# Kernel tuning notes

Hardware: AMD Instinct MI355X
Metric: run time of the kernel (lower is better)

## Reference

```python
import jax, jax.numpy as jnp
import numpy as np

K, A, DIM = 1024, 16384, 512


def setup_inputs() -> dict:
    key = jax.random.key(0)
    ks = jax.random.split(key, 8)
    B, H, W = 2048, 8, 8
    z_t = jax.random.randint(ks[0], (B, H, W), 0, K, dtype=jnp.int64)
    z_tp1 = jax.random.randint(ks[1], (B, H, W), 0, K, dtype=jnp.int64)
    embed_w = jax.random.normal(ks[2], (K, DIM), dtype=jnp.float32) * 0.02
    # MLP: Linear(2*dim -> dim), GELU, Linear(dim -> dim)
    lim1 = 1.0 / np.sqrt(2 * DIM)
    w1 = jax.random.uniform(ks[3], (2 * DIM, DIM), minval=-lim1, maxval=lim1, dtype=jnp.float32)
    b1 = jax.random.uniform(ks[4], (DIM,), minval=-lim1, maxval=lim1, dtype=jnp.float32)
    lim2 = 1.0 / np.sqrt(DIM)
    w2 = jax.random.uniform(ks[5], (DIM, DIM), minval=-lim2, maxval=lim2, dtype=jnp.float32)
    b2 = jax.random.uniform(ks[6], (DIM,), minval=-lim2, maxval=lim2, dtype=jnp.float32)
    codebook_w = jax.random.normal(ks[7], (A, DIM), dtype=jnp.float32) * 0.02
    return {"z_t": z_t, "z_tp1": z_tp1, "embed_w": embed_w, "w1": w1, "b1": b1,
            "w2": w2, "b2": b2, "codebook_w": codebook_w}


def reference(z_t, z_tp1, embed_w, w1, b1, w2, b2, codebook_w):
    B = z_t.shape[0]
    # embed int code grids and mean-pool over H*W tokens -> [B, dim]
    e_t = embed_w[z_t.reshape(B, -1)].mean(axis=1)
    e_tp1 = embed_w[z_tp1.reshape(B, -1)].mean(axis=1)
    h = jnp.concatenate([e_t, e_tp1], axis=-1)          # [B, 2*dim]
    h = jax.nn.gelu(h @ w1 + b1, approximate=False)
    e = h @ w2 + b2                                      # [B, dim]
    # VQ: squared L2 distance to each code, argmin, gather
    d2 = (jnp.sum(e * e, axis=1, keepdims=True)
          - 2.0 * e @ codebook_w.T
          + jnp.sum(codebook_w * codebook_w, axis=1)[None, :])  # [B, A]
    ids = jnp.argmin(d2, axis=1)                         # [B]
    q = codebook_w[ids]                                  # [B, dim]
    return ids, q
```

## Files before the change

kernel.cpp:

```cpp
#include <hip/hip_runtime.h>
#include <hip/hip_bf16.h>

#define TOK 64
#define DIMC 512

typedef __attribute__((ext_vector_type(8))) short v8s;
typedef __attribute__((ext_vector_type(4))) float v4f;

__device__ __forceinline__ unsigned int f2ord(float f) {
  unsigned int u = __float_as_uint(f);
  return (u & 0x80000000u) ? ~u : (u | 0x80000000u);
}

__device__ __forceinline__ float gelu_exact(float x) {
  return 0.5f * x * (1.0f + erff(x * 0.70710678118654752440f));
}

__device__ __forceinline__ unsigned short f2bf(float x) {
  unsigned int u = __float_as_uint(x);
  return (unsigned short)((u + 0x7FFFu + ((u >> 16) & 1u)) >> 16);
}
__device__ __forceinline__ float bf2f(unsigned short h) {
  return __uint_as_float((unsigned int)h << 16);
}

__device__ __forceinline__ void gl2lds16(const void* g, void* l) {
  __builtin_amdgcn_global_load_lds((const __attribute__((address_space(1))) void*)g,
                                   (__attribute__((address_space(3))) void*)l,
                                   16, 0, 0);
}

__global__ __launch_bounds__(256) void k_embed(const int* __restrict__ zt,
                                               const int* __restrict__ ztp,
                                               const float* __restrict__ emb,
                                               unsigned short* __restrict__ hh,
                                               unsigned short* __restrict__ hl,
                                               unsigned long long* __restrict__ rowmin) {
  const int b = blockIdx.x;
  const int tid = threadIdx.x;
  __shared__ int codes[128];
  if (tid < 64) codes[tid] = zt[b * TOK + tid];
  else if (tid < 128) codes[tid] = ztp[b * TOK + (tid - 64)];
  if (tid == 0) rowmin[b] = 0xFFFFFFFFFFFFFFFFull;
  __syncthreads();
  const int half = tid >> 7;
  const int c4 = tid & 127;
  const float4* emb4 = (const float4*)emb;
  float4 s = make_float4(0.f, 0.f, 0.f, 0.f);
  #pragma unroll 8
  for (int t = 0; t < TOK; t++) {
    const int code = codes[half * TOK + t];
    const float4 v = emb4[code * 128 + c4];
    s.x += v.x; s.y += v.y; s.z += v.z; s.w += v.w;
  }
  const float inv = 1.0f / 64.0f;
  float f[4] = {s.x * inv, s.y * inv, s.z * inv, s.w * inv};
  unsigned short hi[4], lo[4];
  #pragma unroll
  for (int i = 0; i < 4; i++) {
    hi[i] = f2bf(f[i]);
    lo[i] = f2bf(f[i] - bf2f(hi[i]));
  }
  const int off = b * 1024 + half * 512 + c4 * 4;
  *(ushort4*)&hh[off] = make_ushort4(hi[0], hi[1], hi[2], hi[3]);
  *(ushort4*)&hl[off] = make_ushort4(lo[0], lo[1], lo[2], lo[3]);
}

__global__ __launch_bounds__(256) void k_wprep(const float* __restrict__ w,
                                               unsigned short* __restrict__ wth,
                                               unsigned short* __restrict__ wtl,
                                               int Kd, int N) {
  __shared__ float t[32][33];
  const int k0 = blockIdx.x * 32, n0 = blockIdx.y * 32;
  const int c = threadIdx.x & 31, r = threadIdx.x >> 5;
  #pragma unroll
  for (int i = 0; i < 4; i++)
    t[r + i * 8][c] = w[(size_t)(k0 + r + i * 8) * N + n0 + c];
  __syncthreads();
  #pragma unroll
  for (int i = 0; i < 4; i++) {
    const float v = t[c][r + i * 8];
    const unsigned short hi = f2bf(v);
    const unsigned short lo = f2bf(v - bf2f(hi));
    wth[(size_t)(n0 + r + i * 8) * Kd + k0 + c] = hi;
    wtl[(size_t)(n0 + r + i * 8) * Kd + k0 + c] = lo;
  }
}

template <bool GELU>
__global__ __launch_bounds__(256) void k_gemm(const unsigned short* __restrict__ Ah_,
                                              const unsigned short* __restrict__ Al_,
                                              const unsigned short* __restrict__ Bh_,
                                              const unsigned short* __restrict__ Bl_,
                                              const float* __restrict__ bias,
                                              unsigned short* __restrict__ oh,
                                              unsigned short* __restrict__ ol,
                                              int Kd, int N) {
  __shared__ unsigned short Ahs[64 * 32];
  __shared__ unsigned short Als[64 * 32];
  __shared__ unsigned short Bhs[64 * 32];
  __shared__ unsigned short Bls[64 * 32];

  const int tid = threadIdx.x;
  const int lane = tid & 63;
  const int wid = tid >> 6;
  const int m0 = blockIdx.x * 64;
  const int n0 = blockIdx.y * 64;

  v4f acc[2][2];
  #pragma unroll
  for (int i = 0; i < 2; i++)
    #pragma unroll
    for (int j = 0; j < 2; j++) acc[i][j] = (v4f)(0.f);

  const unsigned short* gsrc;
  unsigned short* ldst;
  if (wid == 0)      { gsrc = Ah_ + (size_t)m0 * Kd; ldst = Ahs; }
  else if (wid == 1) { gsrc = Al_ + (size_t)m0 * Kd; ldst = Als; }
  else if (wid == 2) { gsrc = Bh_ + (size_t)n0 * Kd; ldst = Bhs; }
  else               { gsrc = Bl_ + (size_t)n0 * Kd; ldst = Bls; }

  const int srow = lane >> 2;
  const int sk = (lane & 3) * 8;
  const int wm = wid >> 1, wn = wid & 1;
  const int fr = lane & 15;
  const int fq = (lane >> 4) * 8;

  for (int k0 = 0; k0 < Kd; k0 += 32) {
    __syncthreads();
    #pragma unroll
    for (int j = 0; j < 4; j++)
      gl2lds16(gsrc + (size_t)(j * 16 + srow) * Kd + k0 + sk, ldst + j * 512);
    __syncthreads();

    v8s ah[2], al[2], bh[2], bl[2];
    #pragma unroll
    for (int t = 0; t < 2; t++) {
      const int ar = (wm * 32 + t * 16 + fr) * 32 + fq;
      const int br = (wn * 32 + t * 16 + fr) * 32 + fq;
      ah[t] = *(const v8s*)&Ahs[ar];
      al[t] = *(const v8s*)&Als[ar];
      bh[t] = *(const v8s*)&Bhs[br];
      bl[t] = *(const v8s*)&Bls[br];
    }
    #pragma unroll
    for (int mt = 0; mt < 2; mt++)
      #pragma unroll
      for (int nt = 0; nt < 2; nt++) {
        acc[mt][nt] = __builtin_amdgcn_mfma_f32_16x16x32_bf16(ah[mt], bh[nt], acc[mt][nt], 0, 0, 0);
        acc[mt][nt] = __builtin_amdgcn_mfma_f32_16x16x32_bf16(ah[mt], bl[nt], acc[mt][nt], 0, 0, 0);
        acc[mt][nt] = __builtin_amdgcn_mfma_f32_16x16x32_bf16(al[mt], bh[nt], acc[mt][nt], 0, 0, 0);
      }
  }

  const int col16 = lane & 15;
  const int q = lane >> 4;
  int colv[2]; float bv[2];
  #pragma unroll
  for (int nt = 0; nt < 2; nt++) {
    colv[nt] = n0 + wn * 32 + nt * 16 + col16;
    bv[nt] = bias[colv[nt]];
  }
  #pragma unroll
  for (int mt = 0; mt < 2; mt++)
    #pragma unroll
    for (int reg = 0; reg < 4; reg++) {
      const int row = m0 + wm * 32 + mt * 16 + q * 4 + reg;
      #pragma unroll
      for (int nt = 0; nt < 2; nt++) {
        float v = acc[mt][nt][reg] + bv[nt];
        if (GELU) v = gelu_exact(v);
        const unsigned short hi = f2bf(v);
        oh[(size_t)row * N + colv[nt]] = hi;
        ol[(size_t)row * N + colv[nt]] = f2bf(v - bf2f(hi));
      }
    }
}

__global__ __launch_bounds__(256) void k_cbprep(const float* __restrict__ cb,
                                                unsigned short* __restrict__ ch,
                                                unsigned short* __restrict__ cl,
                                                float* __restrict__ cnorm) {
  const int row = blockIdx.x * 4 + (threadIdx.x >> 6);
  const int lane = threadIdx.x & 63;
  const float4* cb4 = (const float4*)cb;
  const float4 va = cb4[row * 128 + lane * 2];
  const float4 vb = cb4[row * 128 + lane * 2 + 1];
  float s = va.x * va.x + va.y * va.y + va.z * va.z + va.w * va.w
          + vb.x * vb.x + vb.y * vb.y + vb.z * vb.z + vb.w * vb.w;
  float f[8] = {va.x, va.y, va.z, va.w, vb.x, vb.y, vb.z, vb.w};
  unsigned short hi[8], lo[8];
  #pragma unroll
  for (int i = 0; i < 8; i++) {
    hi[i] = f2bf(f[i]);
    lo[i] = f2bf(f[i] - bf2f(hi[i]));
  }
  ushort4* chp = (ushort4*)&ch[row * DIMC + lane * 8];
  ushort4* clp = (ushort4*)&cl[row * DIMC + lane * 8];
  chp[0] = make_ushort4(hi[0], hi[1], hi[2], hi[3]);
  chp[1] = make_ushort4(hi[4], hi[5], hi[6], hi[7]);
  clp[0] = make_ushort4(lo[0], lo[1], lo[2], lo[3]);
  clp[1] = make_ushort4(lo[4], lo[5], lo[6], lo[7]);
  #pragma unroll
  for (int off = 32; off > 0; off >>= 1) s += __shfl_down(s, off);
  if (lane == 0) cnorm[row] = s;
}

__global__ __launch_bounds__(256, 2) void k_vq(const unsigned short* __restrict__ eh,
                                               const unsigned short* __restrict__ el,
                                               const unsigned short* __restrict__ ch,
                                               const unsigned short* __restrict__ cl,
                                               const float* __restrict__ cnorm,
                                               unsigned long long* __restrict__ rowmin) {
  __shared__ unsigned short Ah[128 * 32];
  __shared__ unsigned short Al[128 * 32];
  __shared__ unsigned short Bh[128 * 32];
  __shared__ unsigned short Bl[128 * 32];

  const int tid = threadIdx.x;
  const int lane = tid & 63;
  const int wid = tid >> 6;
  const int r0 = blockIdx.x * 128;
  const int c0 = blockIdx.y * 128;

  v4f acc[4][4];
  #pragma unroll
  for (int i = 0; i < 4; i++)
    #pragma unroll
    for (int j = 0; j < 4; j++) acc[i][j] = (v4f)(0.f);

  const int lrow = lane >> 2;
  const int lk = (lane & 3) * 8;
  const unsigned short* gsrc;
  unsigned short* ldst;
  if (wid == 0)      { gsrc = eh + (size_t)r0 * DIMC; ldst = Ah; }
  else if (wid == 1) { gsrc = el + (size_t)r0 * DIMC; ldst = Al; }
  else if (wid == 2) { gsrc = ch + (size_t)c0 * DIMC; ldst = Bh; }
  else               { gsrc = cl + (size_t)c0 * DIMC; ldst = Bl; }

  const int wm = wid >> 1;
  const int wn = wid & 1;
  const int fr = lane & 15;
  const int fq = (lane >> 4) * 8;

  for (int k0 = 0; k0 < DIMC; k0 += 32) {
    __syncthreads();
    #pragma unroll
    for (int j = 0; j < 8; j++)
      gl2lds16(gsrc + (size_t)(j * 16 + lrow) * DIMC + k0 + lk, ldst + j * 512);
    __syncthreads();

    v8s ahf[4], alf[4], bhf[4], blf[4];
    #pragma unroll
    for (int t = 0; t < 4; t++) {
      const int ar = (wm * 64 + t * 16 + fr) * 32 + fq;
      const int br = (wn * 64 + t * 16 + fr) * 32 + fq;
      ahf[t] = *(const v8s*)&Ah[ar];
      alf[t] = *(const v8s*)&Al[ar];
      bhf[t] = *(const v8s*)&Bh[br];
      blf[t] = *(const v8s*)&Bl[br];
    }
    #pragma unroll
    for (int mt = 0; mt < 4; mt++)
      #pragma unroll
      for (int nt = 0; nt < 4; nt++) {
        acc[mt][nt] = __builtin_amdgcn_mfma_f32_16x16x32_bf16(ahf[mt], bhf[nt], acc[mt][nt], 0, 0, 0);
        acc[mt][nt] = __builtin_amdgcn_mfma_f32_16x16x32_bf16(ahf[mt], blf[nt], acc[mt][nt], 0, 0, 0);
        acc[mt][nt] = __builtin_amdgcn_mfma_f32_16x16x32_bf16(alf[mt], bhf[nt], acc[mt][nt], 0, 0, 0);
      }
  }

  const int col16 = lane & 15;
  const int q = lane >> 4;
  float cn[4];
  #pragma unroll
  for (int nt = 0; nt < 4; nt++) cn[nt] = cnorm[c0 + wn * 64 + nt * 16 + col16];

  #pragma unroll
  for (int mt = 0; mt < 4; mt++) {
    #pragma unroll
    for (int reg = 0; reg < 4; reg++) {
      const int row = r0 + wm * 64 + mt * 16 + q * 4 + reg;
      float best = fmaf(-2.f, acc[mt][0][reg], cn[0]);
      int bid = c0 + wn * 64 + col16;
      #pragma unroll
      for (int nt = 1; nt < 4; nt++) {
        const float s = fmaf(-2.f, acc[mt][nt][reg], cn[nt]);
        const int id = c0 + wn * 64 + nt * 16 + col16;
        if (s < best) { best = s; bid = id; }
      }
      unsigned long long v =
          ((unsigned long long)f2ord(best) << 32) | (unsigned int)bid;
      #pragma unroll
      for (int off = 8; off > 0; off >>= 1) {
        const unsigned long long o = __shfl_down(v, off, 16);
        if (o < v) v = o;
      }
      if (col16 == 0) atomicMin(&rowmin[row], v);
    }
  }
}

__global__ __launch_bounds__(64) void k_final(const unsigned long long* __restrict__ rowmin,
                                              const float* __restrict__ cb,
                                              float* __restrict__ out,
                                              int B) {
  const int b = blockIdx.x;
  const int t = threadIdx.x;
  const unsigned long long m = rowmin[b];
  const int id = (int)(unsigned int)(m & 0xFFFFFFFFull);
  if (t == 0) out[b] = (float)id;
  float4* q4 = (float4*)(out + B) + b * 128;
  const float4* cb4 = (const float4*)cb + (size_t)id * 128;
  q4[t] = cb4[t];
  q4[t + 64] = cb4[t + 64];
}

extern "C" void kernel_launch(void* const* d_in, const int* in_sizes, int n_in,
                              void* d_out, int out_size, void* d_ws, size_t ws_size,
                              hipStream_t stream) {
  const int* zt = (const int*)d_in[0];
  const int* ztp = (const int*)d_in[1];
  const float* emb = (const float*)d_in[2];
  const float* w1 = (const float*)d_in[3];
  const float* b1 = (const float*)d_in[4];
  const float* w2 = (const float*)d_in[5];
  const float* b2 = (const float*)d_in[6];
  const float* cb = (const float*)d_in[7];
  float* out = (float*)d_out;

  const int B = in_sizes[0] / TOK;
  const int A = in_sizes[7] / DIMC;

  char* p = (char*)d_ws;
  unsigned short* hh = (unsigned short*)p;  p += (size_t)B * 1024 * 2;
  unsigned short* hl = (unsigned short*)p;  p += (size_t)B * 1024 * 2;
  unsigned short* w1th = (unsigned short*)p; p += (size_t)512 * 1024 * 2;
  unsigned short* w1tl = (unsigned short*)p; p += (size_t)512 * 1024 * 2;
  unsigned short* w2th = (unsigned short*)p; p += (size_t)512 * 512 * 2;
  unsigned short* w2tl = (unsigned short*)p; p += (size_t)512 * 512 * 2;
  unsigned short* h1h = (unsigned short*)p; p += (size_t)B * DIMC * 2;
  unsigned short* h1l = (unsigned short*)p; p += (size_t)B * DIMC * 2;
  unsigned short* eh = (unsigned short*)p;  p += (size_t)B * DIMC * 2;
  unsigned short* el = (unsigned short*)p;  p += (size_t)B * DIMC * 2;
  unsigned short* ch = (unsigned short*)p;  p += (size_t)A * DIMC * 2;
  unsigned short* cl = (unsigned short*)p;  p += (size_t)A * DIMC * 2;
  float* cnorm = (float*)p;                 p += (size_t)A * 4;
  unsigned long long* rowmin = (unsigned long long*)p;

  k_embed<<<B, 256, 0, stream>>>(zt, ztp, emb, hh, hl, rowmin);
  k_wprep<<<dim3(1024 / 32, 512 / 32), 256, 0, stream>>>(w1, w1th, w1tl, 1024, 512);
  k_wprep<<<dim3(512 / 32, 512 / 32), 256, 0, stream>>>(w2, w2th, w2tl, 512, 512);
  k_cbprep<<<A / 4, 256, 0, stream>>>(cb, ch, cl, cnorm);
  k_gemm<true><<<dim3(B / 64, 512 / 64), 256, 0, stream>>>(hh, hl, w1th, w1tl, b1, h1h, h1l, 1024, 512);
  k_gemm<false><<<dim3(B / 64, 512 / 64), 256, 0, stream>>>(h1h, h1l, w2th, w2tl, b2, eh, el, 512, 512);
  dim3 vq_grid(B / 128, A / 128);
  k_vq<<<vq_grid, 256, 0, stream>>>(eh, el, ch, cl, cnorm, rowmin);
  k_final<<<B, 64, 0, stream>>>(rowmin, cb, out, B);
}
```

Before: 251.8 us.

## Merge prep kernels into one launch and swizzle VQ block order for L2 reuse

```diff
diff --git a/kernel.cpp b/kernel.cpp
--- a/kernel.cpp
+++ b/kernel.cpp
@@ -30,60 +30,97 @@
                                    16, 0, 0);
 }
 
-__global__ __launch_bounds__(256) void k_embed(const int* __restrict__ zt,
-                                               const int* __restrict__ ztp,
-                                               const float* __restrict__ emb,
-                                               unsigned short* __restrict__ hh,
-                                               unsigned short* __restrict__ hl,
-                                               unsigned long long* __restrict__ rowmin) {
-  const int b = blockIdx.x;
+__global__ __launch_bounds__(256) void k_prep(
+    const int* __restrict__ zt, const int* __restrict__ ztp,
+    const float* __restrict__ emb,
+    unsigned short* __restrict__ hh, unsigned short* __restrict__ hl,
+    unsigned long long* __restrict__ rowmin,
+    const float* __restrict__ w1, unsigned short* __restrict__ w1th,
+    unsigned short* __restrict__ w1tl,
+    const float* __restrict__ w2, unsigned short* __restrict__ w2th,
+    unsigned short* __restrict__ w2tl,
+    const float* __restrict__ cb, unsigned short* __restrict__ ch,
+    unsigned short* __restrict__ cl, float* __restrict__ cnorm) {
+  __shared__ int codes[128];
+  __shared__ float tbuf[32][33];
+  const int bid = blockIdx.x;
   const int tid = threadIdx.x;
-  __shared__ int codes[128];
-  if (tid < 64) codes[tid] = zt[b * TOK + tid];
-  else if (tid < 128) codes[tid] = ztp[b * TOK + (tid - 64)];
-  if (tid == 0) rowmin[b] = 0xFFFFFFFFFFFFFFFFull;
-  __syncthreads();
-  const int half = tid >> 7;
-  const int c4 = tid & 127;
-  const float4* emb4 = (const float4*)emb;
-  float4 s = make_float4(0.f, 0.f, 0.f, 0.f);
-  #pragma unroll 8
-  for (int t = 0; t < TOK; t++) {
-    const int code = codes[half * TOK + t];
-    const float4 v = emb4[code * 128 + c4];
-    s.x += v.x; s.y += v.y; s.z += v.z; s.w += v.w;
-  }
-  const float inv = 1.0f / 64.0f;
-  float f[4] = {s.x * inv, s.y * inv, s.z * inv, s.w * inv};
-  unsigned short hi[4], lo[4];
-  #pragma unroll
-  for (int i = 0; i < 4; i++) {
-    hi[i] = f2bf(f[i]);
-    lo[i] = f2bf(f[i] - bf2f(hi[i]));
-  }
-  const int off = b * 1024 + half * 512 + c4 * 4;
-  *(ushort4*)&hh[off] = make_ushort4(hi[0], hi[1], hi[2], hi[3]);
-  *(ushort4*)&hl[off] = make_ushort4(lo[0], lo[1], lo[2], lo[3]);
-}
-
-__global__ __launch_bounds__(256) void k_wprep(const float* __restrict__ w,
-                                               unsigned short* __restrict__ wth,
-                                               unsigned short* __restrict__ wtl,
-                                               int Kd, int N) {
-  __shared__ float t[32][33];
-  const int k0 = blockIdx.x * 32, n0 = blockIdx.y * 32;
-  const int c = threadIdx.x & 31, r = threadIdx.x >> 5;
-  #pragma unroll
-  for (int i = 0; i < 4; i++)
-    t[r + i * 8][c] = w[(size_t)(k0 + r + i * 8) * N + n0 + c];
-  __syncthreads();
-  #pragma unroll
-  for (int i = 0; i < 4; i++) {
-    const float v = t[c][r + i * 8];
-    const unsigned short hi = f2bf(v);
-    const unsigned short lo = f2bf(v - bf2f(hi));
-    wth[(size_t)(n0 + r + i * 8) * Kd + k0 + c] = hi;
-    wtl[(size_t)(n0 + r + i * 8) * Kd + k0 + c] = lo;
+
+  if (bid < 2048) {
+    const int b = bid;
+    if (tid < 64) codes[tid] = zt[b * TOK + tid];
+    else if (tid < 128) codes[tid] = ztp[b * TOK + (tid - 64)];
+    if (tid == 0) rowmin[b] = 0xFFFFFFFFFFFFFFFFull;
+    __syncthreads();
+    const int half = tid >> 7;
+    const int c4 = tid & 127;
+    const float4* emb4 = (const float4*)emb;
+    float4 s = make_float4(0.f, 0.f, 0.f, 0.f);
+    #pragma unroll 8
+    for (int t = 0; t < TOK; t++) {
+      const int code = codes[half * TOK + t];
+      const float4 v = emb4[code * 128 + c4];
+      s.x += v.x; s.y += v.y; s.z += v.z; s.w += v.w;
+    }
+    const float inv = 1.0f / 64.0f;
+    float f[4] = {s.x * inv, s.y * inv, s.z * inv, s.w * inv};
+    unsigned short hi[4], lo[4];
+    #pragma unroll
+    for (int i = 0; i < 4; i++) {
+      hi[i] = f2bf(f[i]);
+      lo[i] = f2bf(f[i] - bf2f(hi[i]));
+    }
+    const int off = b * 1024 + half * 512 + c4 * 4;
+    *(ushort4*)&hh[off] = make_ushort4(hi[0], hi[1], hi[2], hi[3]);
+    *(ushort4*)&hl[off] = make_ushort4(lo[0], lo[1], lo[2], lo[3]);
+  } else if (bid < 2816) {
+    const float* w; unsigned short *wth, *wtl; int Kd, N, k0, n0;
+    if (bid < 2560) {
+      const int i = bid - 2048;
+      w = w1; wth = w1th; wtl = w1tl; Kd = 1024; N = 512;
+      k0 = (i & 31) * 32; n0 = (i >> 5) * 32;
+    } else {
+      const int i = bid - 2560;
+      w = w2; wth = w2th; wtl = w2tl; Kd = 512; N = 512;
+      k0 = (i & 15) * 32; n0 = (i >> 4) * 32;
+    }
+    const int c = tid & 31, r = tid >> 5;
+    #pragma unroll
+    for (int i = 0; i < 4; i++)
+      tbuf[r + i * 8][c] = w[(size_t)(k0 + r + i * 8) * N + n0 + c];
+    __syncthreads();
+    #pragma unroll
+    for (int i = 0; i < 4; i++) {
+      const float v = tbuf[c][r + i * 8];
+      const unsigned short hi = f2bf(v);
+      const unsigned short lo = f2bf(v - bf2f(hi));
+      wth[(size_t)(n0 + r + i * 8) * Kd + k0 + c] = hi;
+      wtl[(size_t)(n0 + r + i * 8) * Kd + k0 + c] = lo;
+    }
+  } else {
+    const int row = (bid - 2816) * 4 + (tid >> 6);
+    const int lane = tid & 63;
+    const float4* cb4 = (const float4*)cb;
+    const float4 va = cb4[row * 128 + lane * 2];
+    const float4 vb = cb4[row * 128 + lane * 2 + 1];
+    float s = va.x * va.x + va.y * va.y + va.z * va.z + va.w * va.w
+            + vb.x * vb.x + vb.y * vb.y + vb.z * vb.z + vb.w * vb.w;
+    float f[8] = {va.x, va.y, va.z, va.w, vb.x, vb.y, vb.z, vb.w};
+    unsigned short hi[8], lo[8];
+    #pragma unroll
+    for (int i = 0; i < 8; i++) {
+      hi[i] = f2bf(f[i]);
+      lo[i] = f2bf(f[i] - bf2f(hi[i]));
+    }
+    ushort4* chp = (ushort4*)&ch[row * DIMC + lane * 8];
+    ushort4* clp = (ushort4*)&cl[row * DIMC + lane * 8];
+    chp[0] = make_ushort4(hi[0], hi[1], hi[2], hi[3]);
+    chp[1] = make_ushort4(hi[4], hi[5], hi[6], hi[7]);
+    clp[0] = make_ushort4(lo[0], lo[1], lo[2], lo[3]);
+    clp[1] = make_ushort4(lo[4], lo[5], lo[6], lo[7]);
+    #pragma unroll
+    for (int off = 32; off > 0; off >>= 1) s += __shfl_down(s, off);
+    if (lane == 0) cnorm[row] = s;
   }
 }
 
@@ -177,35 +214,6 @@
     }
 }
 
-__global__ __launch_bounds__(256) void k_cbprep(const float* __restrict__ cb,
-                                                unsigned short* __restrict__ ch,
-                                                unsigned short* __restrict__ cl,
-                                                float* __restrict__ cnorm) {
-  const int row = blockIdx.x * 4 + (threadIdx.x >> 6);
-  const int lane = threadIdx.x & 63;
-  const float4* cb4 = (const float4*)cb;
-  const float4 va = cb4[row * 128 + lane * 2];
-  const float4 vb = cb4[row * 128 + lane * 2 + 1];
-  float s = va.x * va.x + va.y * va.y + va.z * va.z + va.w * va.w
-          + vb.x * vb.x + vb.y * vb.y + vb.z * vb.z + vb.w * vb.w;
-  float f[8] = {va.x, va.y, va.z, va.w, vb.x, vb.y, vb.z, vb.w};
-  unsigned short hi[8], lo[8];
-  #pragma unroll
-  for (int i = 0; i < 8; i++) {
-    hi[i] = f2bf(f[i]);
-    lo[i] = f2bf(f[i] - bf2f(hi[i]));
-  }
-  ushort4* chp = (ushort4*)&ch[row * DIMC + lane * 8];
-  ushort4* clp = (ushort4*)&cl[row * DIMC + lane * 8];
-  chp[0] = make_ushort4(hi[0], hi[1], hi[2], hi[3]);
-  chp[1] = make_ushort4(hi[4], hi[5], hi[6], hi[7]);
-  clp[0] = make_ushort4(lo[0], lo[1], lo[2], lo[3]);
-  clp[1] = make_ushort4(lo[4], lo[5], lo[6], lo[7]);
-  #pragma unroll
-  for (int off = 32; off > 0; off >>= 1) s += __shfl_down(s, off);
-  if (lane == 0) cnorm[row] = s;
-}
-
 __global__ __launch_bounds__(256, 2) void k_vq(const unsigned short* __restrict__ eh,
                                                const unsigned short* __restrict__ el,
                                                const unsigned short* __restrict__ ch,
@@ -220,14 +228,18 @@
   const int tid = threadIdx.x;
   const int lane = tid & 63;
   const int wid = tid >> 6;
-  const int r0 = blockIdx.x * 128;
-  const int c0 = blockIdx.y * 128;
+  const int bid = blockIdx.x;
+  const int j = bid >> 3;
+  const int x = j & 15;
+  const int y = ((j >> 4) << 3) | (bid & 7);
+  const int r0 = x * 128;
+  const int c0 = y * 128;
 
   v4f acc[4][4];
   #pragma unroll
   for (int i = 0; i < 4; i++)
     #pragma unroll
-    for (int j = 0; j < 4; j++) acc[i][j] = (v4f)(0.f);
+    for (int jj = 0; jj < 4; jj++) acc[i][jj] = (v4f)(0.f);
 
   const int lrow = lane >> 2;
   const int lk = (lane & 3) * 8;
@@ -246,8 +258,8 @@
   for (int k0 = 0; k0 < DIMC; k0 += 32) {
     __syncthreads();
     #pragma unroll
-    for (int j = 0; j < 8; j++)
-      gl2lds16(gsrc + (size_t)(j * 16 + lrow) * DIMC + k0 + lk, ldst + j * 512);
+    for (int jj = 0; jj < 8; jj++)
+      gl2lds16(gsrc + (size_t)(jj * 16 + lrow) * DIMC + k0 + lk, ldst + jj * 512);
     __syncthreads();
 
     v8s ahf[4], alf[4], bhf[4], blf[4];
@@ -282,15 +294,15 @@
     for (int reg = 0; reg < 4; reg++) {
       const int row = r0 + wm * 64 + mt * 16 + q * 4 + reg;
       float best = fmaf(-2.f, acc[mt][0][reg], cn[0]);
-      int bid = c0 + wn * 64 + col16;
+      int bid2 = c0 + wn * 64 + col16;
       #pragma unroll
       for (int nt = 1; nt < 4; nt++) {
         const float s = fmaf(-2.f, acc[mt][nt][reg], cn[nt]);
         const int id = c0 + wn * 64 + nt * 16 + col16;
-        if (s < best) { best = s; bid = id; }
+        if (s < best) { best = s; bid2 = id; }
       }
       unsigned long long v =
-          ((unsigned long long)f2ord(best) << 32) | (unsigned int)bid;
+          ((unsigned long long)f2ord(best) << 32) | (unsigned int)bid2;
       #pragma unroll
       for (int off = 8; off > 0; off >>= 1) {
         const unsigned long long o = __shfl_down(v, off, 16);
@@ -348,13 +360,11 @@
   float* cnorm = (float*)p;                 p += (size_t)A * 4;
   unsigned long long* rowmin = (unsigned long long*)p;
 
-  k_embed<<<B, 256, 0, stream>>>(zt, ztp, emb, hh, hl, rowmin);
-  k_wprep<<<dim3(1024 / 32, 512 / 32), 256, 0, stream>>>(w1, w1th, w1tl, 1024, 512);
-  k_wprep<<<dim3(512 / 32, 512 / 32), 256, 0, stream>>>(w2, w2th, w2tl, 512, 512);
-  k_cbprep<<<A / 4, 256, 0, stream>>>(cb, ch, cl, cnorm);
+  k_prep<<<2816 + A / 4, 256, 0, stream>>>(zt, ztp, emb, hh, hl, rowmin,
+                                           w1, w1th, w1tl, w2, w2th, w2tl,
+                                           cb, ch, cl, cnorm);
   k_gemm<true><<<dim3(B / 64, 512 / 64), 256, 0, stream>>>(hh, hl, w1th, w1tl, b1, h1h, h1l, 1024, 512);
   k_gemm<false><<<dim3(B / 64, 512 / 64), 256, 0, stream>>>(h1h, h1l, w2th, w2tl, b2, eh, el, 512, 512);
-  dim3 vq_grid(B / 128, A / 128);
-  k_vq<<<vq_grid, 256, 0, stream>>>(eh, el, ch, cl, cnorm, rowmin);
+  k_vq<<<(B / 128) * (A / 128), 256, 0, stream>>>(eh, el, ch, cl, cnorm, rowmin);
   k_final<<<B, 64, 0, stream>>>(rowmin, cb, out, B);
 }
```

New measurement: 242.9 us. -3.5%, faster.
